# Performance work log

Measured on AMD Instinct MI355X. Metric: run time of the kernel, lower is better.

Reference implementation:

```python
import jax, jax.numpy as jnp
import numpy as np

NMS_THR = 0.5
SCORE_THR = 0.05
MAX_BOXES = 300
N_ANCHORS = 5000
N_CLASSES = 80
IMG = 640.0  # image size used to scale synthetic box coords


def setup_inputs() -> dict:
    key = jax.random.key(0)
    k1, k2, k3 = jax.random.split(key, 3)
    # build well-formed boxes (x1<=x2, y1<=y2) in a 640x640 image
    c1 = jax.random.uniform(k1, (1, N_ANCHORS, 2), jnp.float32) * IMG
    c2 = jax.random.uniform(k2, (1, N_ANCHORS, 2), jnp.float32) * IMG
    boxes = jnp.concatenate([jnp.minimum(c1, c2), jnp.maximum(c1, c2) + 1.0], axis=-1)
    # classification scores in [0,1], squared to skew toward low values like sigmoid logits
    classification = jax.random.uniform(k3, (1, N_ANCHORS, N_CLASSES), jnp.float32) ** 2
    return {"boxes": boxes, "classification": classification}


def _iou_matrix(b):
    # b: [N,4] as (x1,y1,x2,y2) -> [N,N] pairwise IoU
    x1, y1, x2, y2 = b[:, 0], b[:, 1], b[:, 2], b[:, 3]
    area = (x2 - x1) * (y2 - y1)
    iw = jnp.maximum(jnp.minimum(x2[:, None], x2[None, :]) - jnp.maximum(x1[:, None], x1[None, :]), 0.0)
    ih = jnp.maximum(jnp.minimum(y2[:, None], y2[None, :]) - jnp.maximum(y1[:, None], y1[None, :]), 0.0)
    inter = iw * ih
    union = area[:, None] + area[None, :] - inter
    return inter / jnp.maximum(union, 1e-8)


def _nms_one_class(scores, iou):
    # greedy NMS for one class; scores: [N], iou: [N,N] (shared across classes)
    n = scores.shape[0]
    order = jnp.argsort(-scores)          # descending score order
    valid = scores > SCORE_THR            # per-class score-threshold filter
    idxs = jnp.arange(n)

    def step(carry, oi):
        suppressed, kept, count = carry
        alive = (~suppressed[oi]) & valid[oi] & (count < MAX_BOXES)
        # a kept box suppresses all others with IoU above threshold
        suppressed = suppressed | (alive & (iou[oi] > NMS_THR) & (idxs != oi))
        kept = kept.at[oi].set(alive)
        return (suppressed, kept, count + alive.astype(jnp.int32)), None

    init = (jnp.zeros(n, jnp.bool_), jnp.zeros(n, jnp.bool_), jnp.int32(0))
    (_, kept, _), _ = jax.lax.scan(step, init, order)
    return kept  # [N] bool mask in original index space


def reference(boxes, classification):
    b = boxes[0]             # [N,4]
    cls = classification[0]  # [N,C]
    iou = _iou_matrix(b)     # [N,N], class-independent
    kept = jax.vmap(_nms_one_class, in_axes=(1, None))(cls, iou)  # [C,N]
    # scatter surviving scores back to dense per-class score map (zeros elsewhere)
    selected = jnp.where(kept.T, cls, 0.0)                        # [N,C]
    detections = jnp.concatenate([b, selected], axis=1)           # [N,4+C]
    return detections[None]                                       # [1,N,4+C]
```

## Files before the change

kernel.cpp:

```cpp
#include <hip/hip_runtime.h>

#define N_ANCHORS 5000
#define N_CLASSES 80
#define OUT_COLS  84
#define MAX_BOXES 300
#define SCORE_THR 0.05f

#define SORT_PAD  5056
#define NB        4096
#define BLOCK     1024
#define SLOTS     8
#define DONEP     0x40000000

typedef unsigned long long u64;
typedef unsigned int u32;

#define WG __HIP_MEMORY_SCOPE_WORKGROUP

__device__ __forceinline__ float readlane_f(float v, int l) {
    return __int_as_float(__builtin_amdgcn_readlane(__float_as_int(v), l));
}
__device__ __forceinline__ u32 aload(u32* p) {
    return __hip_atomic_load(p, __ATOMIC_ACQUIRE, WG);
}
__device__ __forceinline__ int bucket_of(float s) {
    float u = sqrtf(s);
    int b = (int)((u - 0.2236f) * 5275.0f);
    return min(max(b, 0), NB - 1);
}
__device__ __forceinline__ bool iou_q(float4 a, float aa, float4 q) {
    float iw = fmaxf(fminf(a.z, q.z) - fmaxf(a.x, q.x), 0.0f);
    float ih = fmaxf(fminf(a.w, q.w) - fmaxf(a.y, q.y), 0.0f);
    float aq = (q.z - q.x) * (q.w - q.y);
    return 3.0f * (iw * ih) > aa + aq;
}

#define INIT_BLKS 1641
#define TR_BX     157
#define TR_BY     3
#define TR_BLKS   (TR_BX * TR_BY)

__global__ __launch_bounds__(256) void prep(const float* __restrict__ boxes,
                                            const float* __restrict__ cls,
                                            float* __restrict__ clsT,
                                            float* __restrict__ out) {
    __shared__ float tile[32][33];
    int b = blockIdx.x;
    if (b < INIT_BLKS) {
        int i = b * 256 + threadIdx.x;
        if (i < N_ANCHORS * OUT_COLS) {
            int row = i / OUT_COLS, col = i - row * OUT_COLS;
            out[i] = (col < 4) ? boxes[row * 4 + col] : 0.0f;
        }
        return;
    }
    b -= INIT_BLKS;
    int bx_ = b % TR_BX, by_ = b / TR_BX;
    int j0 = bx_ * 32, c0 = by_ * 32;
    int tx = threadIdx.x & 31, ty = threadIdx.x >> 5;
    #pragma unroll
    for (int r = 0; r < 32; r += 8) {
        int j = j0 + ty + r, c = c0 + tx;
        tile[ty + r][tx] = (j < N_ANCHORS && c < N_CLASSES) ? cls[j * N_CLASSES + c] : 0.0f;
    }
    __syncthreads();
    #pragma unroll
    for (int r = 0; r < 32; r += 8) {
        int c = c0 + ty + r, j = j0 + tx;
        if (c < N_CLASSES && j < N_ANCHORS) clsT[(size_t)c * N_ANCHORS + j] = tile[tx][ty + r];
    }
}

__global__ __launch_bounds__(BLOCK, 1) void nms(const float* __restrict__ clsT,
                                                const float4* __restrict__ boxes4,
                                                float* __restrict__ out) {
    __shared__ __align__(16) char SMEM[62208];
    u64*    lk    = (u64*)SMEM;
    u32*    hist  = (u32*)(SMEM + 40448);
    u64*    Iring = (u64*)(SMEM + 40448);
    float4* Bring = (float4*)(SMEM + 44544);
    u64*    kout  = (u64*)(SMEM + 52736);
    float4* kbox  = (float4*)(SMEM + 56832);
    u64*    KS    = (u64*)(SMEM + 61952);
    u32*    wtot  = (u32*)(SMEM + 62016);
    u32*    KBa   = (u32*)(SMEM + 62080);
    u32*    flagI = (u32*)(SMEM + 62112);
    u32*    flagK = (u32*)(SMEM + 62144);
    u32*    prog  = (u32*)(SMEM + 62176);
    u32*    kcnt  = (u32*)(SMEM + 62180);

    const int c = blockIdx.x;
    const int t = threadIdx.x;
    const int lane = t & 63;
    const int wv = t >> 6;

    const float4* cp4 = (const float4*)(clsT + (size_t)c * N_ANCHORS);
    u32 sb[8];
    #pragma unroll
    for (int m = 0; m < 2; ++m) {
        int vi = m * 1024 + t;
        float4 v = make_float4(0.f, 0.f, 0.f, 0.f);
        if (vi < N_ANCHORS / 4) v = cp4[vi];
        sb[m * 4 + 0] = (v.x > SCORE_THR) ? __float_as_uint(v.x) : 0u;
        sb[m * 4 + 1] = (v.y > SCORE_THR) ? __float_as_uint(v.y) : 0u;
        sb[m * 4 + 2] = (v.z > SCORE_THR) ? __float_as_uint(v.z) : 0u;
        sb[m * 4 + 3] = (v.w > SCORE_THR) ? __float_as_uint(v.w) : 0u;
    }
    for (int b = t; b < NB; b += BLOCK) hist[b] = 0u;
    if (t < 320) kbox[t] = make_float4(1e9f, 1e9f, 1e9f, 1e9f);
    if (t < SLOTS) { flagI[t] = 0u; flagK[t] = 0u; }
    if (t == 0) { *prog = 0u; *kcnt = 0u; }
    __syncthreads();
    #pragma unroll
    for (int m = 0; m < 8; ++m)
        if (sb[m]) atomicAdd(&hist[bucket_of(__uint_as_float(sb[m]))], 1u);
    __syncthreads();

    const int hbase = t * 4;
    u32 vals[4]; u32 run = 0;
    #pragma unroll
    for (int k = 0; k < 4; ++k) { run += hist[hbase + k]; vals[k] = run; }
    u32 x = run;
    #pragma unroll
    for (int off = 1; off < 64; off <<= 1) { u32 y = __shfl_up(x, off); if (lane >= off) x += y; }
    if (lane == 63) wtot[wv] = x;
    __syncthreads();
    u32 woff = 0;
    for (int w = 0; w < wv; ++w) woff += wtot[w];
    const u32 exb = woff + x - run;
    #pragma unroll
    for (int k = 0; k < 4; ++k) hist[hbase + k] = exb + (k ? vals[k - 1] : 0u);
    __syncthreads();
    #pragma unroll
    for (int m = 0; m < 8; ++m) {
        if (sb[m]) {
            int j = ((m >> 2) * 1024 + t) * 4 + (m & 3);
            u32 pos = atomicAdd(&hist[bucket_of(__uint_as_float(sb[m]))], 1u);
            lk[pos] = ((u64)sb[m] << 32) | (u32)(~(u32)j);
        }
    }
    __syncthreads();
    const int total = (int)hist[NB - 1];
    for (int v = total + t; v < SORT_PAD; v += BLOCK) lk[v] = 0ull;
    for (int b = hbase; b < hbase + 4; ++b) {
        int s0 = b ? (int)hist[b - 1] : 0;
        int e  = (int)hist[b];
        for (int i = s0 + 1; i < e; ++i) {
            u64 key = lk[i]; int q = i - 1;
            while (q >= s0 && lk[q] < key) { lk[q + 1] = lk[q]; --q; }
            lk[q + 1] = key;
        }
    }
    __syncthreads();
    const int nch = (total + 63) >> 6;

    if (wv >= 1 && wv <= 4) {
        for (int j = wv - 1; j < nch; j += 4) {
            const int slot = j & (SLOTS - 1);
            u64 e = lk[j * 64 + lane];
            u32 jj = e ? ~(u32)e : 0u;
            float4 bx = boxes4[jj];
            float ar = (bx.z - bx.x) * (bx.w - bx.y);
            u32 p;
            for (;;) {
                p = aload(prog);
                if ((int)p >= j - (SLOTS - 1)) break;
                __builtin_amdgcn_s_sleep(2);
            }
            if (p >= DONEP) return;
            u64 word = 0ull;
            #pragma unroll 16
            for (int q = 0; q < 64; ++q) {
                float4 o;
                o.x = readlane_f(bx.x, q); o.y = readlane_f(bx.y, q);
                o.z = readlane_f(bx.z, q); o.w = readlane_f(bx.w, q);
                if (iou_q(bx, ar, o)) word |= (1ull << q);
            }
            Iring[slot * 64 + lane] = word;
            if (lane == 0)
                __hip_atomic_store(&flagI[slot], (u32)(j + 1), __ATOMIC_RELEASE, WG);
        }
        return;
    }
    if (wv >= 5) {
        for (int j = wv - 5; j < nch; j += 11) {
            const int slot = j & (SLOTS - 1);
            u64 e = lk[j * 64 + lane];
            bool validL = (e != 0ull);
            u32 jj = validL ? ~(u32)e : 0u;
            float4 bx = boxes4[jj];
            float ar = (bx.z - bx.x) * (bx.w - bx.y);
            u32 p;
            for (;;) {
                p = aload(prog);
                if ((int)p >= j - (SLOTS - 1)) break;
                __builtin_amdgcn_s_sleep(2);
            }
            if (p >= DONEP) return;
            Bring[slot * 64 + lane] = bx;
            u64 vm = __ballot(validL);
            u64 ks = ~vm;
            u32 ka = aload(kcnt);
            const int ng = (int)((ka + 63) >> 6);

            if (ka) {
                float4 kb[5];
                #pragma unroll
                for (int g = 0; g < 5; ++g)
                    kb[g] = (g < ng) ? kbox[g * 64 + lane]
                                     : make_float4(1e9f, 1e9f, 1e9f, 1e9f);
                for (int i = 0; i < 64; ++i) {
                    if (!((vm >> i) & 1ull)) continue;
                    float cx1 = readlane_f(bx.x, i), cy1 = readlane_f(bx.y, i);
                    float cx2 = readlane_f(bx.z, i), cy2 = readlane_f(bx.w, i);
                    float car = (cx2 - cx1) * (cy2 - cy1);
                    bool found = false;
                    #pragma unroll
                    for (int g = 0; g < 5; ++g) {
                        if (!found && g < ng) {
                            float iw = fmaxf(fminf(cx2, kb[g].z) - fmaxf(cx1, kb[g].x), 0.0f);
                            float ih = fmaxf(fminf(cy2, kb[g].w) - fmaxf(cy1, kb[g].y), 0.0f);
                            float aq = (kb[g].z - kb[g].x) * (kb[g].w - kb[g].y);
                            bool s = 3.0f * (iw * ih) > car + aq;
                            found = (__ballot(s) != 0ull);
                        }
                    }
                    if (found) ks |= (1ull << i);
                }
            }
            bool sup = (ks >> lane) & 1ull;

            for (;;) {
                p = aload(prog);
                if ((int)p >= j - 2) break;
                __builtin_amdgcn_s_sleep(1);
            }
            u32 kb2 = (p >= DONEP) ? ka : aload(kcnt);
            if (kb2 < ka) kb2 = ka;
            u32 r1 = (kb2 + 3) & ~3u;
            for (u32 r = ka & ~3u; r < r1; r += 4) {
                float4 q0 = kbox[r + 0], q1 = kbox[r + 1], q2 = kbox[r + 2], q3 = kbox[r + 3];
                bool s = iou_q(bx, ar, q0) | iou_q(bx, ar, q1) | iou_q(bx, ar, q2) | iou_q(bx, ar, q3);
                sup = sup || s;
            }
            u64 ksf = __ballot(sup);
            if (lane == 0) {
                KS[slot] = ksf; KBa[slot] = kb2;
                __hip_atomic_store(&flagK[slot], (u32)(j + 1), __ATOMIC_RELEASE, WG);
            }
            if (p >= DONEP) return;
        }
        return;
    }

    int kept = 0; u32 kcur = 0; bool capped = false;
    for (int k = 0; k < nch; ++k) {
        const int slot = k & (SLOTS - 1);
        u64 key = lk[k * 64 + lane];
        bool valid = (key != 0ull);
        u32 j = valid ? ~(u32)key : 0u;
        float sc = __uint_as_float((u32)(key >> 32));

        while (aload(&flagK[slot]) != (u32)(k + 1)) { }
        u64 ks = KS[slot];
        if (ks != ~0ull) {
            u32 kb = KBa[slot];
            float4 bx = Bring[slot * 64 + lane];
            float ar = (bx.z - bx.x) * (bx.w - bx.y);
            bool alive = valid && !((ks >> lane) & 1ull);
            u32 r1 = (kcur + 3) & ~3u;
            for (u32 r = kb & ~3u; r < r1; r += 4) {
                float4 q0 = kbox[r + 0], q1 = kbox[r + 1], q2 = kbox[r + 2], q3 = kbox[r + 3];
                bool s = iou_q(bx, ar, q0) | iou_q(bx, ar, q1) | iou_q(bx, ar, q2) | iou_q(bx, ar, q3);
                alive = alive && !s;
            }
            u64 rem = __ballot(alive);
            if (rem) {
                while (aload(&flagI[slot]) != (u32)(k + 1)) { }
                u64 I = Iring[slot * 64 + lane];
                u64 km = 0ull;
                while (rem) {
                    int pos = __ffsll((long long)rem) - 1;
                    km |= 1ull << pos;
                    if (++kept == MAX_BOXES) { capped = true; break; }
                    u32 lo = (u32)__builtin_amdgcn_readlane((int)(u32)I, pos);
                    u32 hi = (u32)__builtin_amdgcn_readlane((int)(u32)(I >> 32), pos);
                    rem &= ~(((u64)hi << 32) | (u64)lo);
                }
                if ((km >> lane) & 1ull) {
                    int rank = (int)__popcll(km & ((1ull << lane) - 1ull));
                    kbox[kcur + rank] = bx;
                    kout[kcur + rank] = ((u64)__float_as_uint(sc) << 32) | j;
                }
                kcur += (u32)__popcll(km);
            }
        }
        if (capped) break;
        if (lane == 0) {
            __hip_atomic_store(kcnt, kcur, __ATOMIC_RELEASE, WG);
            __hip_atomic_store(prog, (u32)(k + 1), __ATOMIC_RELEASE, WG);
        }
    }
    if (lane == 0) __hip_atomic_store(prog, (u32)DONEP, __ATOMIC_RELEASE, WG);

    for (u32 i = (u32)lane; i < kcur; i += 64) {
        u64 e = kout[i];
        out[(size_t)((u32)e) * OUT_COLS + 4 + c] = __uint_as_float((u32)(e >> 32));
    }
}

extern "C" void kernel_launch(void* const* d_in, const int* in_sizes, int n_in,
                              void* d_out, int out_size, void* d_ws, size_t ws_size,
                              hipStream_t stream) {
    const float* boxes = (const float*)d_in[0];
    const float* cls   = (const float*)d_in[1];
    float* out = (float*)d_out;
    float* clsT = (float*)d_ws;

    prep<<<INIT_BLKS + TR_BLKS, 256, 0, stream>>>(boxes, cls, clsT, out);
    nms<<<N_CLASSES, BLOCK, 0, stream>>>(clsT, (const float4*)boxes, out);
}
```

Before: 139.5 us.

## Fuse prep into NMS kernel, cache kept-box areas, rebalance IoU/suppress warps

Removes the separate prep kernel: each class block reads its scores directly with strided loads and writes its own output column zeros, with blocks 0-3 copying box coordinates. It also stores kept-box areas in shared memory so IoU tests skip recomputing them, and moves the warp split from 4/11 to 6/9 IoU/suppression warps. The suppression warps now do a simple linear scan over kept boxes with a periodic early exit instead of the per-box ballot loop. The bucket order is flipped so descending scores come from the histogram directly, and the main warp waits on the IoU ring unconditionally. The gains are one less launch and cheaper inner loops; the cost is uncoalesced strided score reads and output writes spread across 80 blocks.

```diff
diff --git a/kernel.cpp b/kernel.cpp
--- a/kernel.cpp
+++ b/kernel.cpp
@@ -11,6 +11,8 @@
 #define BLOCK     1024
 #define SLOTS     8
 #define DONEP     0x40000000
+#define NIW       6
+#define NSW       9
 
 typedef unsigned long long u64;
 typedef unsigned int u32;
@@ -26,93 +28,59 @@
 __device__ __forceinline__ int bucket_of(float s) {
     float u = sqrtf(s);
     int b = (int)((u - 0.2236f) * 5275.0f);
-    return min(max(b, 0), NB - 1);
-}
-__device__ __forceinline__ bool iou_q(float4 a, float aa, float4 q) {
+    return (NB - 1) - min(max(b, 0), NB - 1);
+}
+__device__ __forceinline__ bool iou3(float4 a, float aa, float4 q, float aq) {
     float iw = fmaxf(fminf(a.z, q.z) - fmaxf(a.x, q.x), 0.0f);
     float ih = fmaxf(fminf(a.w, q.w) - fmaxf(a.y, q.y), 0.0f);
-    float aq = (q.z - q.x) * (q.w - q.y);
     return 3.0f * (iw * ih) > aa + aq;
 }
 
-#define INIT_BLKS 1641
-#define TR_BX     157
-#define TR_BY     3
-#define TR_BLKS   (TR_BX * TR_BY)
-
-__global__ __launch_bounds__(256) void prep(const float* __restrict__ boxes,
-                                            const float* __restrict__ cls,
-                                            float* __restrict__ clsT,
-                                            float* __restrict__ out) {
-    __shared__ float tile[32][33];
-    int b = blockIdx.x;
-    if (b < INIT_BLKS) {
-        int i = b * 256 + threadIdx.x;
-        if (i < N_ANCHORS * OUT_COLS) {
-            int row = i / OUT_COLS, col = i - row * OUT_COLS;
-            out[i] = (col < 4) ? boxes[row * 4 + col] : 0.0f;
-        }
-        return;
-    }
-    b -= INIT_BLKS;
-    int bx_ = b % TR_BX, by_ = b / TR_BX;
-    int j0 = bx_ * 32, c0 = by_ * 32;
-    int tx = threadIdx.x & 31, ty = threadIdx.x >> 5;
-    #pragma unroll
-    for (int r = 0; r < 32; r += 8) {
-        int j = j0 + ty + r, c = c0 + tx;
-        tile[ty + r][tx] = (j < N_ANCHORS && c < N_CLASSES) ? cls[j * N_CLASSES + c] : 0.0f;
-    }
-    __syncthreads();
-    #pragma unroll
-    for (int r = 0; r < 32; r += 8) {
-        int c = c0 + ty + r, j = j0 + tx;
-        if (c < N_CLASSES && j < N_ANCHORS) clsT[(size_t)c * N_ANCHORS + j] = tile[tx][ty + r];
-    }
-}
-
-__global__ __launch_bounds__(BLOCK, 1) void nms(const float* __restrict__ clsT,
+__global__ __launch_bounds__(BLOCK, 1) void nms(const float* __restrict__ cls,
                                                 const float4* __restrict__ boxes4,
                                                 float* __restrict__ out) {
-    __shared__ __align__(16) char SMEM[62208];
+    __shared__ __align__(16) char SMEM[63168];
     u64*    lk    = (u64*)SMEM;
     u32*    hist  = (u32*)(SMEM + 40448);
     u64*    Iring = (u64*)(SMEM + 40448);
     float4* Bring = (float4*)(SMEM + 44544);
     u64*    kout  = (u64*)(SMEM + 52736);
     float4* kbox  = (float4*)(SMEM + 56832);
-    u64*    KS    = (u64*)(SMEM + 61952);
-    u32*    wtot  = (u32*)(SMEM + 62016);
-    u32*    KBa   = (u32*)(SMEM + 62080);
-    u32*    flagI = (u32*)(SMEM + 62112);
-    u32*    flagK = (u32*)(SMEM + 62144);
-    u32*    prog  = (u32*)(SMEM + 62176);
-    u32*    kcnt  = (u32*)(SMEM + 62180);
+    float*  karea = (float*)(SMEM + 61696);
+    u64*    KS    = (u64*)(SMEM + 62912);
+    u32*    wtot  = (u32*)(SMEM + 62976);
+    u32*    KBa   = (u32*)(SMEM + 63040);
+    u32*    flagI = (u32*)(SMEM + 63072);
+    u32*    flagK = (u32*)(SMEM + 63104);
+    u32*    prog  = (u32*)(SMEM + 63136);
+    u32*    kcnt  = (u32*)(SMEM + 63140);
 
     const int c = blockIdx.x;
     const int t = threadIdx.x;
     const int lane = t & 63;
     const int wv = t >> 6;
-
-    const float4* cp4 = (const float4*)(clsT + (size_t)c * N_ANCHORS);
-    u32 sb[8];
-    #pragma unroll
-    for (int m = 0; m < 2; ++m) {
-        int vi = m * 1024 + t;
-        float4 v = make_float4(0.f, 0.f, 0.f, 0.f);
-        if (vi < N_ANCHORS / 4) v = cp4[vi];
-        sb[m * 4 + 0] = (v.x > SCORE_THR) ? __float_as_uint(v.x) : 0u;
-        sb[m * 4 + 1] = (v.y > SCORE_THR) ? __float_as_uint(v.y) : 0u;
-        sb[m * 4 + 2] = (v.z > SCORE_THR) ? __float_as_uint(v.z) : 0u;
-        sb[m * 4 + 3] = (v.w > SCORE_THR) ? __float_as_uint(v.w) : 0u;
-    }
+    const float* boxesf = (const float*)boxes4;
+
+    u32 sb[5];
+    #pragma unroll
+    for (int m = 0; m < 5; ++m) {
+        int j = m * BLOCK + t;
+        float v = (j < N_ANCHORS) ? cls[(size_t)j * N_CLASSES + c] : 0.0f;
+        sb[m] = (v > SCORE_THR) ? __float_as_uint(v) : 0u;
+    }
+    for (int i = t; i < N_ANCHORS; i += BLOCK)
+        out[(size_t)i * OUT_COLS + 4 + c] = 0.0f;
+    if (c < 4)
+        for (int i = t; i < N_ANCHORS; i += BLOCK)
+            out[(size_t)i * OUT_COLS + c] = boxesf[(size_t)i * 4 + c];
+
     for (int b = t; b < NB; b += BLOCK) hist[b] = 0u;
-    if (t < 320) kbox[t] = make_float4(1e9f, 1e9f, 1e9f, 1e9f);
+    if (t < 304) { kbox[t] = make_float4(1e9f, 1e9f, 1e9f, 1e9f); karea[t] = 1e18f; }
     if (t < SLOTS) { flagI[t] = 0u; flagK[t] = 0u; }
     if (t == 0) { *prog = 0u; *kcnt = 0u; }
     __syncthreads();
     #pragma unroll
-    for (int m = 0; m < 8; ++m)
+    for (int m = 0; m < 5; ++m)
         if (sb[m]) atomicAdd(&hist[bucket_of(__uint_as_float(sb[m]))], 1u);
     __syncthreads();
 
@@ -132,9 +100,9 @@
     for (int k = 0; k < 4; ++k) hist[hbase + k] = exb + (k ? vals[k - 1] : 0u);
     __syncthreads();
     #pragma unroll
-    for (int m = 0; m < 8; ++m) {
+    for (int m = 0; m < 5; ++m) {
         if (sb[m]) {
-            int j = ((m >> 2) * 1024 + t) * 4 + (m & 3);
+            int j = m * BLOCK + t;
             u32 pos = atomicAdd(&hist[bucket_of(__uint_as_float(sb[m]))], 1u);
             lk[pos] = ((u64)sb[m] << 32) | (u32)(~(u32)j);
         }
@@ -154,8 +122,8 @@
     __syncthreads();
     const int nch = (total + 63) >> 6;
 
-    if (wv >= 1 && wv <= 4) {
-        for (int j = wv - 1; j < nch; j += 4) {
+    if (wv >= 1 && wv <= NIW) {
+        for (int j = wv - 1; j < nch; j += NIW) {
             const int slot = j & (SLOTS - 1);
             u64 e = lk[j * 64 + lane];
             u32 jj = e ? ~(u32)e : 0u;
@@ -174,7 +142,10 @@
                 float4 o;
                 o.x = readlane_f(bx.x, q); o.y = readlane_f(bx.y, q);
                 o.z = readlane_f(bx.z, q); o.w = readlane_f(bx.w, q);
-                if (iou_q(bx, ar, o)) word |= (1ull << q);
+                float aq = readlane_f(ar, q);
+                float iw = fmaxf(fminf(bx.z, o.z) - fmaxf(bx.x, o.x), 0.0f);
+                float ih = fmaxf(fminf(bx.w, o.w) - fmaxf(bx.y, o.y), 0.0f);
+                if (3.0f * (iw * ih) > ar + aq) word |= (1ull << q);
             }
             Iring[slot * 64 + lane] = word;
             if (lane == 0)
@@ -182,8 +153,8 @@
         }
         return;
     }
-    if (wv >= 5) {
-        for (int j = wv - 5; j < nch; j += 11) {
+    if (wv > NIW) {
+        for (int j = wv - (NIW + 1); j < nch; j += NSW) {
             const int slot = j & (SLOTS - 1);
             u64 e = lk[j * 64 + lane];
             bool validL = (e != 0ull);
@@ -198,38 +169,15 @@
             }
             if (p >= DONEP) return;
             Bring[slot * 64 + lane] = bx;
-            u64 vm = __ballot(validL);
-            u64 ks = ~vm;
+            bool sup = !validL;
             u32 ka = aload(kcnt);
-            const int ng = (int)((ka + 63) >> 6);
-
-            if (ka) {
-                float4 kb[5];
-                #pragma unroll
-                for (int g = 0; g < 5; ++g)
-                    kb[g] = (g < ng) ? kbox[g * 64 + lane]
-                                     : make_float4(1e9f, 1e9f, 1e9f, 1e9f);
-                for (int i = 0; i < 64; ++i) {
-                    if (!((vm >> i) & 1ull)) continue;
-                    float cx1 = readlane_f(bx.x, i), cy1 = readlane_f(bx.y, i);
-                    float cx2 = readlane_f(bx.z, i), cy2 = readlane_f(bx.w, i);
-                    float car = (cx2 - cx1) * (cy2 - cy1);
-                    bool found = false;
-                    #pragma unroll
-                    for (int g = 0; g < 5; ++g) {
-                        if (!found && g < ng) {
-                            float iw = fmaxf(fminf(cx2, kb[g].z) - fmaxf(cx1, kb[g].x), 0.0f);
-                            float ih = fmaxf(fminf(cy2, kb[g].w) - fmaxf(cy1, kb[g].y), 0.0f);
-                            float aq = (kb[g].z - kb[g].x) * (kb[g].w - kb[g].y);
-                            bool s = 3.0f * (iw * ih) > car + aq;
-                            found = (__ballot(s) != 0ull);
-                        }
-                    }
-                    if (found) ks |= (1ull << i);
-                }
-            }
-            bool sup = (ks >> lane) & 1ull;
-
+            for (u32 r = 0; r < ka; r += 4) {
+                float4 q0 = kbox[r], q1 = kbox[r + 1], q2 = kbox[r + 2], q3 = kbox[r + 3];
+                float4 a4 = *(const float4*)(karea + r);
+                sup = sup | iou3(bx, ar, q0, a4.x) | iou3(bx, ar, q1, a4.y)
+                          | iou3(bx, ar, q2, a4.z) | iou3(bx, ar, q3, a4.w);
+                if ((r & 28u) == 28u && !__ballot(!sup)) break;
+            }
             for (;;) {
                 p = aload(prog);
                 if ((int)p >= j - 2) break;
@@ -239,9 +187,10 @@
             if (kb2 < ka) kb2 = ka;
             u32 r1 = (kb2 + 3) & ~3u;
             for (u32 r = ka & ~3u; r < r1; r += 4) {
-                float4 q0 = kbox[r + 0], q1 = kbox[r + 1], q2 = kbox[r + 2], q3 = kbox[r + 3];
-                bool s = iou_q(bx, ar, q0) | iou_q(bx, ar, q1) | iou_q(bx, ar, q2) | iou_q(bx, ar, q3);
-                sup = sup || s;
+                float4 q0 = kbox[r], q1 = kbox[r + 1], q2 = kbox[r + 2], q3 = kbox[r + 3];
+                float4 a4 = *(const float4*)(karea + r);
+                sup = sup | iou3(bx, ar, q0, a4.x) | iou3(bx, ar, q1, a4.y)
+                          | iou3(bx, ar, q2, a4.z) | iou3(bx, ar, q3, a4.w);
             }
             u64 ksf = __ballot(sup);
             if (lane == 0) {
@@ -262,22 +211,24 @@
         float sc = __uint_as_float((u32)(key >> 32));
 
         while (aload(&flagK[slot]) != (u32)(k + 1)) { }
+        while (aload(&flagI[slot]) != (u32)(k + 1)) { }
         u64 ks = KS[slot];
         if (ks != ~0ull) {
             u32 kb = KBa[slot];
             float4 bx = Bring[slot * 64 + lane];
+            u64 I = Iring[slot * 64 + lane];
             float ar = (bx.z - bx.x) * (bx.w - bx.y);
             bool alive = valid && !((ks >> lane) & 1ull);
             u32 r1 = (kcur + 3) & ~3u;
             for (u32 r = kb & ~3u; r < r1; r += 4) {
-                float4 q0 = kbox[r + 0], q1 = kbox[r + 1], q2 = kbox[r + 2], q3 = kbox[r + 3];
-                bool s = iou_q(bx, ar, q0) | iou_q(bx, ar, q1) | iou_q(bx, ar, q2) | iou_q(bx, ar, q3);
+                float4 q0 = kbox[r], q1 = kbox[r + 1], q2 = kbox[r + 2], q3 = kbox[r + 3];
+                float4 a4 = *(const float4*)(karea + r);
+                bool s = iou3(bx, ar, q0, a4.x) | iou3(bx, ar, q1, a4.y)
+                       | iou3(bx, ar, q2, a4.z) | iou3(bx, ar, q3, a4.w);
                 alive = alive && !s;
             }
             u64 rem = __ballot(alive);
             if (rem) {
-                while (aload(&flagI[slot]) != (u32)(k + 1)) { }
-                u64 I = Iring[slot * 64 + lane];
                 u64 km = 0ull;
                 while (rem) {
                     int pos = __ffsll((long long)rem) - 1;
@@ -290,6 +241,7 @@
                 if ((km >> lane) & 1ull) {
                     int rank = (int)__popcll(km & ((1ull << lane) - 1ull));
                     kbox[kcur + rank] = bx;
+                    karea[kcur + rank] = ar;
                     kout[kcur + rank] = ((u64)__float_as_uint(sc) << 32) | j;
                 }
                 kcur += (u32)__popcll(km);
@@ -312,11 +264,7 @@
 extern "C" void kernel_launch(void* const* d_in, const int* in_sizes, int n_in,
                               void* d_out, int out_size, void* d_ws, size_t ws_size,
                               hipStream_t stream) {
-    const float* boxes = (const float*)d_in[0];
-    const float* cls   = (const float*)d_in[1];
+    const float* cls = (const float*)d_in[1];
     float* out = (float*)d_out;
-    float* clsT = (float*)d_ws;
-
-    prep<<<INIT_BLKS + TR_BLKS, 256, 0, stream>>>(boxes, cls, clsT, out);
-    nms<<<N_CLASSES, BLOCK, 0, stream>>>(clsT, (const float4*)boxes, out);
-}
+    nms<<<N_CLASSES, BLOCK, 0, stream>>>(cls, (const float4*)d_in[0], out);
+}
```

New measurement: 147.2 us. 1.05x slower.
